# Kernel optimization log

Hardware: AMD Instinct MI355X
Metric: run time of the kernel (lower is better)

Reference implementation:

```python
import jax, jax.numpy as jnp
import numpy as np

T, B = 512, 256
OBS, H = 64, 512
M1, M2 = 512, 256


def setup_inputs() -> dict:
    key = jax.random.key(0)
    k = jax.random.split(key, 10)
    n = lambda i, shape, s=1.0: jax.random.normal(k[i], shape, dtype=jnp.float32) * s
    return {
        "x": n(0, (T * B, OBS)),
        "done": (jax.random.uniform(k[1], (T * B,)) < 0.05).astype(jnp.float32),
        "h0": n(2, (1, B, H), 0.1),
        "c0": n(3, (1, B, H), 0.1),
        "W_ih": n(4, (4 * H, OBS), OBS ** -0.5),
        "W_hh": n(5, (4 * H, H), H ** -0.5),
        "b_ih": jnp.zeros((4 * H,), jnp.float32),
        "b_hh": jnp.zeros((4 * H,), jnp.float32),
        "ln_g": jnp.ones((H,), jnp.float32),
        "ln_b": jnp.zeros((H,), jnp.float32),
        "W1": n(6, (M1, H), H ** -0.5),
        "b1": jnp.zeros((M1,), jnp.float32),
        "W2": n(7, (M2, M1), M1 ** -0.5),
        "b2": jnp.zeros((M2,), jnp.float32),
        "Wv": n(8, (1, M2), M2 ** -0.5),
        "bv": jnp.zeros((1,), jnp.float32),
    }


def _forward(x, done, h0, c0, W_ih, W_hh, b_ih, b_hh, ln_g, ln_b, W1, b1, W2, b2, Wv, bv):
    Bsz = h0.shape[1]
    obs = W_ih.shape[1]
    xs = x.reshape(-1, Bsz, obs)   # [T, B, obs]
    ds = done.reshape(-1, Bsz)     # [T, B]

    def step(carry, td):
        h, c = carry
        xt, dt = td
        m = (1.0 - dt)[:, None]    # done-based state reset, as in LSTMwithDones
        h = h * m
        c = c * m
        gates = xt @ W_ih.T + b_ih + h @ W_hh.T + b_hh  # [B, 4H]
        i, f, g, o = jnp.split(gates, 4, axis=-1)       # torch gate order i,f,g,o
        c = jax.nn.sigmoid(f) * c + jax.nn.sigmoid(i) * jnp.tanh(g)
        h = jax.nn.sigmoid(o) * jnp.tanh(c)
        return (h, c), h

    (hT, cT), hs = jax.lax.scan(step, (h0[0], c0[0]), (xs, ds))
    hidden = hs.reshape(-1, hs.shape[-1])  # flatten(cat(new_hidden), 0, 1) -> [T*B, H]

    # LayerNorm (eps = 1e-5, torch default)
    mu = hidden.mean(-1, keepdims=True)
    var = ((hidden - mu) ** 2).mean(-1, keepdims=True)
    hidden = (hidden - mu) * jax.lax.rsqrt(var + 1e-5) * ln_g + ln_b

    # MLP with tanh activation after every Linear (build_mlp appends act each layer)
    hmlp = jnp.tanh(hidden @ W1.T + b1)
    hmlp = jnp.tanh(hmlp @ W2.T + b2)
    value = hmlp @ Wv.T + bv               # [T*B, 1]
    return value, hT[None], cT[None]


def reference(x, done, h0, c0, W_ih, W_hh, b_ih, b_hh, ln_g, ln_b, W1, b1, W2, b2, Wv, bv):
    return _forward(x, done, h0, c0, W_ih, W_hh, b_ih, b_hh, ln_g, ln_b, W1, b1, W2, b2, Wv, bv)
```

## Files before the change

kernel.cpp:

```cpp
#include <hip/hip_runtime.h>
#include <stdint.h>

constexpr int T_STEPS = 512;
constexpr int BSZ     = 256;
constexpr int OBSD    = 64;
constexpr int HID     = 512;
constexpr int NROWS   = T_STEPS * BSZ;

constexpr int GROUPS = 16;
constexpr int WPG    = 16;
constexpr int BW     = 16;

typedef __attribute__((ext_vector_type(8))) short bf16x8;
typedef __attribute__((ext_vector_type(4))) float f32x4;

__device__ __forceinline__ float bf2f(uint16_t u) {
  union { uint32_t i; float f; } v; v.i = ((uint32_t)u) << 16; return v.f;
}
__device__ __forceinline__ uint16_t f2bf(float f) {
  union { float f; uint32_t i; } v; v.f = f;
  return (uint16_t)((v.i + 0x7FFFu + ((v.i >> 16) & 1u)) >> 16);
}
__device__ __forceinline__ uint64_t pack4(float a, float b, float c, float d) {
  uint32_t lo = (uint32_t)f2bf(a) | ((uint32_t)f2bf(b) << 16);
  uint32_t hi = (uint32_t)f2bf(c) | ((uint32_t)f2bf(d) << 16);
  return (uint64_t)lo | ((uint64_t)hi << 32);
}
__device__ __forceinline__ float sigm(float x) { return 1.f / (1.f + __expf(-x)); }
__device__ __forceinline__ float tanh_fast(float x) {
  float e = __expf(2.f * x);
  return 1.f - 2.f / (e + 1.f);
}

__device__ __forceinline__ void gll16(const void* g, void* l) {
  __builtin_amdgcn_global_load_lds(
      (const __attribute__((address_space(1))) uint32_t*)g,
      (__attribute__((address_space(3))) uint32_t*)l, 16, 0, 0);
}

__global__ __launch_bounds__(256, 1) void lstm_kernel(
    const float* __restrict__ xin, const float* __restrict__ done,
    const float* __restrict__ h0, const float* __restrict__ c0,
    const float* __restrict__ W_ih, const float* __restrict__ W_hh,
    const float* __restrict__ b_ih, const float* __restrict__ b_hh,
    uint16_t* __restrict__ hs, uint32_t* __restrict__ flg,
    float* __restrict__ out)
{
  __shared__ char  Ab[16 * 1152];
  __shared__ float gl[4 * 528];
  __shared__ float bl[128];

  const int wg   = blockIdx.x;
  const int g    = wg & 15;
  const int win  = wg >> 4;
  const int bg   = g * BW;
  const int tid  = threadIdx.x;
  const int lane = tid & 63;
  const int q    = tid >> 6;

  __builtin_amdgcn_fence(__ATOMIC_ACQUIRE, "agent");

  bf16x8 bq0[18], bq1[18];
  {
    const int r0  = q * 512 + win * 32 + (lane & 15);
    const int r1  = r0 + 16;
    const int kg8 = (lane >> 4) * 8;
    #pragma unroll
    for (int ks = 0; ks < 18; ++ks) {
      const float* s0 = (ks < 16)
          ? (W_hh + (size_t)r0 * 512 + ks * 32 + kg8)
          : (W_ih + (size_t)r0 * 64 + (ks - 16) * 32 + kg8);
      const float* s1 = (ks < 16)
          ? (W_hh + (size_t)r1 * 512 + ks * 32 + kg8)
          : (W_ih + (size_t)r1 * 64 + (ks - 16) * 32 + kg8);
      float4 a0 = *(const float4*)s0;
      float4 a1 = *(const float4*)(s0 + 4);
      float4 b0 = *(const float4*)s1;
      float4 b1 = *(const float4*)(s1 + 4);
      bf16x8 va, vb;
      va[0] = (short)f2bf(a0.x); va[1] = (short)f2bf(a0.y);
      va[2] = (short)f2bf(a0.z); va[3] = (short)f2bf(a0.w);
      va[4] = (short)f2bf(a1.x); va[5] = (short)f2bf(a1.y);
      va[6] = (short)f2bf(a1.z); va[7] = (short)f2bf(a1.w);
      vb[0] = (short)f2bf(b0.x); vb[1] = (short)f2bf(b0.y);
      vb[2] = (short)f2bf(b0.z); vb[3] = (short)f2bf(b0.w);
      vb[4] = (short)f2bf(b1.x); vb[5] = (short)f2bf(b1.y);
      vb[6] = (short)f2bf(b1.z); vb[7] = (short)f2bf(b1.w);
      bq0[ks] = va; bq1[ks] = vb;
    }
  }
  if (tid < 128) {
    int gq = tid >> 5, c = tid & 31;
    int grow = gq * 512 + win * 32 + c;
    bl[tid] = b_ih[grow] + b_hh[grow];
  }

  const int b_loc = tid >> 4;
  const int n0    = (tid & 15) * 2;
  float creg0 = c0[(size_t)(bg + b_loc) * HID + win * 32 + n0];
  float creg1 = c0[(size_t)(bg + b_loc) * HID + win * 32 + n0 + 1];

  const int ar  = lane & 15;
  const int kg  = lane >> 4;
  const int rw  = q * 4;

  __syncthreads();

  for (int t = 0; t < T_STEPS; ++t) {
    float dvs[4];
    #pragma unroll
    for (int r8 = 0; r8 < 4; ++r8)
      dvs[r8] = done[(size_t)t * BSZ + bg + rw + r8];
    float dv_b = done[(size_t)t * BSZ + bg + b_loc];

    const float* xrow = xin + ((size_t)t * BSZ + bg + ar) * OBSD + kg * 8;
    float4 x0a = *(const float4*)(xrow);
    float4 x0b = *(const float4*)(xrow + 4);
    float4 x1a = *(const float4*)(xrow + 32);
    float4 x1b = *(const float4*)(xrow + 36);
    bf16x8 xk0, xk1;
    xk0[0] = (short)f2bf(x0a.x); xk0[1] = (short)f2bf(x0a.y);
    xk0[2] = (short)f2bf(x0a.z); xk0[3] = (short)f2bf(x0a.w);
    xk0[4] = (short)f2bf(x0b.x); xk0[5] = (short)f2bf(x0b.y);
    xk0[6] = (short)f2bf(x0b.z); xk0[7] = (short)f2bf(x0b.w);
    xk1[0] = (short)f2bf(x1a.x); xk1[1] = (short)f2bf(x1a.y);
    xk1[2] = (short)f2bf(x1a.z); xk1[3] = (short)f2bf(x1a.w);
    xk1[4] = (short)f2bf(x1b.x); xk1[5] = (short)f2bf(x1b.y);
    xk1[6] = (short)f2bf(x1b.z); xk1[7] = (short)f2bf(x1b.w);

    f32x4 ac0 = {0.f, 0.f, 0.f, 0.f};
    f32x4 ac1 = {0.f, 0.f, 0.f, 0.f};
    ac0 = __builtin_amdgcn_mfma_f32_16x16x32_bf16(xk0, bq0[16], ac0, 0, 0, 0);
    ac1 = __builtin_amdgcn_mfma_f32_16x16x32_bf16(xk0, bq1[16], ac1, 0, 0, 0);
    ac0 = __builtin_amdgcn_mfma_f32_16x16x32_bf16(xk1, bq0[17], ac0, 0, 0, 0);
    ac1 = __builtin_amdgcn_mfma_f32_16x16x32_bf16(xk1, bq1[17], ac1, 0, 0, 0);

    if (t > 0) {
      for (;;) {
        uint32_t f = (lane < WPG)
            ? __hip_atomic_load(flg + g * 64 + q * 16 + lane,
                                __ATOMIC_RELAXED, __HIP_MEMORY_SCOPE_AGENT)
            : 0xFFFFFFFFu;
        if (__all((int)(f >= (uint32_t)t))) break;
      }
      __builtin_amdgcn_fence(__ATOMIC_ACQUIRE, "workgroup");
    }

    if (t == 0) {
      #pragma unroll
      for (int r8 = 0; r8 < 4; ++r8) {
        int r = rw + r8;
        uint64_t v0 = 0, v1 = 0;
        if (dvs[r8] <= 0.5f) {
          const float* hp = h0 + (size_t)(bg + r) * HID;
          float4 ha = *(const float4*)(hp + lane * 4);
          float4 hb = *(const float4*)(hp + 256 + lane * 4);
          v0 = pack4(ha.x, ha.y, ha.z, ha.w);
          v1 = pack4(hb.x, hb.y, hb.z, hb.w);
        }
        *(uint64_t*)(Ab + ((r * 1152 + lane * 8) ^ ((r & 7) << 4))) = v0;
        *(uint64_t*)(Ab + ((r * 1152 + 512 + lane * 8) ^ ((r & 7) << 4))) = v1;
      }
    } else {
      #pragma unroll
      for (int r8 = 0; r8 < 4; ++r8) {
        int r = rw + r8;
        const uint4* hrow =
            (const uint4*)(hs + ((size_t)(t - 1) * BSZ + bg + r) * 512);
        uint4 v = hrow[lane];
        if (dvs[r8] > 0.5f) { v.x = 0; v.y = 0; v.z = 0; v.w = 0; }
        *(uint4*)(Ab + ((r * 1152 + lane * 16) ^ ((r & 7) << 4))) = v;
      }
    }
    __syncthreads();

    #pragma unroll
    for (int ks = 0; ks < 16; ++ks) {
      int kb = ks * 64 + kg * 16;
      bf16x8 a = *(const bf16x8*)(Ab + ((ar * 1152 + kb) ^ ((ar & 7) << 4)));
      ac0 = __builtin_amdgcn_mfma_f32_16x16x32_bf16(a, bq0[ks], ac0, 0, 0, 0);
      ac1 = __builtin_amdgcn_mfma_f32_16x16x32_bf16(a, bq1[ks], ac1, 0, 0, 0);
    }
    {
      int c  = lane & 15;
      int rb = (lane >> 4) * 4;
      #pragma unroll
      for (int r = 0; r < 4; ++r) {
        gl[q * 528 + (rb + r) * 33 + c]      = ac0[r];
        gl[q * 528 + (rb + r) * 33 + 16 + c] = ac1[r];
      }
    }
    __syncthreads();

    {
      float m = dv_b > 0.5f ? 0.f : 1.f;
      float h0v, h1v;
      {
        float I = gl[b_loc * 33 + n0]          + bl[n0];
        float F = gl[528 + b_loc * 33 + n0]    + bl[32 + n0];
        float G = gl[1056 + b_loc * 33 + n0]   + bl[64 + n0];
        float O = gl[1584 + b_loc * 33 + n0]   + bl[96 + n0];
        float cc = creg0 * m;
        cc = sigm(F) * cc + sigm(I) * tanh_fast(G);
        creg0 = cc;
        h0v = sigm(O) * tanh_fast(cc);
      }
      {
        int n1 = n0 + 1;
        float I = gl[b_loc * 33 + n1]          + bl[n1];
        float F = gl[528 + b_loc * 33 + n1]    + bl[32 + n1];
        float G = gl[1056 + b_loc * 33 + n1]   + bl[64 + n1];
        float O = gl[1584 + b_loc * 33 + n1]   + bl[96 + n1];
        float cc = creg1 * m;
        cc = sigm(F) * cc + sigm(I) * tanh_fast(G);
        creg1 = cc;
        h1v = sigm(O) * tanh_fast(cc);
      }
      uint32_t pk = (uint32_t)f2bf(h0v) | ((uint32_t)f2bf(h1v) << 16);
      uint32_t* hp = (uint32_t*)(hs + ((size_t)t * BSZ + bg + b_loc) * HID + win * 32 + n0);
      __hip_atomic_store(hp, pk, __ATOMIC_RELAXED, __HIP_MEMORY_SCOPE_AGENT);
      if (t == T_STEPS - 1) {
        size_t ob = (size_t)(bg + b_loc) * HID + win * 32 + n0;
        out[NROWS + ob]         = h0v;
        out[NROWS + ob + 1]     = h1v;
        out[2 * NROWS + ob]     = creg0;
        out[2 * NROWS + ob + 1] = creg1;
      }
    }
    asm volatile("s_waitcnt vmcnt(0)" ::: "memory");
    if ((tid & 63) == 0)
      __hip_atomic_store(flg + g * 64 + q * 16 + win, (uint32_t)(t + 1),
                         __ATOMIC_RELAXED, __HIP_MEMORY_SCOPE_AGENT);
  }
}

__global__ void prep_kernel(const float* __restrict__ W1, const float* __restrict__ W2,
                            const float* __restrict__ ln_g, const float* __restrict__ ln_b,
                            const float* __restrict__ b1, uint16_t* __restrict__ dst,
                            float* __restrict__ u, float* __restrict__ v)
{
  if (blockIdx.x < 384) {
    int idx = blockIdx.x * 256 + threadIdx.x;
    int i4 = idx * 4;
    float4 val;
    if (i4 < 262144) {
      val = *(const float4*)(W1 + i4);
      int c = i4 & 511;
      float4 gv = *(const float4*)(ln_g + c);
      val.x *= gv.x; val.y *= gv.y; val.z *= gv.z; val.w *= gv.w;
    } else {
      val = *(const float4*)(W2 + (i4 - 262144));
    }
    uint32_t lo = (uint32_t)f2bf(val.x) | ((uint32_t)f2bf(val.y) << 16);
    uint32_t hi = (uint32_t)f2bf(val.z) | ((uint32_t)f2bf(val.w) << 16);
    *(uint64_t*)(dst + i4) = (uint64_t)lo | ((uint64_t)hi << 32);
  } else {
    const int lane = threadIdx.x & 63;
    const int row  = (blockIdx.x - 384) * 4 + (threadIdx.x >> 6);
    const float* wp = W1 + (size_t)row * 512 + lane * 8;
    float4 w0 = *(const float4*)wp;
    float4 w1 = *(const float4*)(wp + 4);
    float4 g0 = *(const float4*)(ln_g + lane * 8);
    float4 g1 = *(const float4*)(ln_g + lane * 8 + 4);
    float4 b0 = *(const float4*)(ln_b + lane * 8);
    float4 b1v = *(const float4*)(ln_b + lane * 8 + 4);
    float su = b0.x * w0.x + b0.y * w0.y + b0.z * w0.z + b0.w * w0.w
             + b1v.x * w1.x + b1v.y * w1.y + b1v.z * w1.z + b1v.w * w1.w;
    float sv = g0.x * w0.x + g0.y * w0.y + g0.z * w0.z + g0.w * w0.w
             + g1.x * w1.x + g1.y * w1.y + g1.z * w1.z + g1.w * w1.w;
    #pragma unroll
    for (int o = 1; o < 64; o <<= 1) { su += __shfl_xor(su, o); sv += __shfl_xor(sv, o); }
    if (lane == 0) { u[row] = su + b1[row]; v[row] = sv; }
  }
}

__global__ __launch_bounds__(256, 2) void gemm1_kernel(
    const uint16_t* __restrict__ Abase, const uint16_t* __restrict__ W,
    uint16_t* __restrict__ C,
    const float* __restrict__ uvec, const float* __restrict__ vvec)
{
  __shared__ uint16_t At[64 * 512];
  __shared__ float sRS[64];
  __shared__ float sMRS[64];
  const int tid  = threadIdx.x;
  const int lane = tid & 63;
  const int wv   = tid >> 6;
  const size_t mbase = (size_t)blockIdx.x * 64;

  for (int r8 = 0; r8 < 16; ++r8) {
    int row = wv * 16 + r8;
    int sb  = (lane * 16) ^ ((row & 7) << 4);
    gll16(Abase + (mbase + row) * 512 + sb / 2, At + row * 512);
  }
  __syncthreads();

  for (int r8 = 0; r8 < 16; ++r8) {
    int row = wv * 16 + r8;
    bf16x8 v = *(const bf16x8*)((const char*)At +
                                ((row * 1024 + lane * 16) ^ ((row & 7) << 4)));
    float s = 0.f, s2 = 0.f;
    #pragma unroll
    for (int j = 0; j < 8; ++j) {
      float f = bf2f((uint16_t)v[j]);
      s += f; s2 += f * f;
    }
    #pragma unroll
    for (int o = 1; o < 64; o <<= 1) {
      s += __shfl_xor(s, o); s2 += __shfl_xor(s2, o);
    }
    if (lane == 0) {
      float mu  = s * (1.f / 512.f);
      float var = s2 * (1.f / 512.f) - mu * mu;
      float rs  = rsqrtf(var + 1e-5f);
      sRS[row]  = rs;
      sMRS[row] = mu * rs;
    }
  }
  __syncthreads();

  const int fr = lane & 15, kg = lane >> 4;
  const int mloc = (wv & 1) * 32;
  const int nhalf = (wv >> 1) * 64;

  for (int nt = 0; nt < 4; ++nt) {
    const int nbase = nt * 128 + nhalf;
    f32x4 vz = {0.f, 0.f, 0.f, 0.f};
    f32x4 acc[4][2];
    #pragma unroll
    for (int i = 0; i < 4; ++i) { acc[i][0] = vz; acc[i][1] = vz; }

    #pragma unroll 4
    for (int kb = 0; kb < 16; ++kb) {
      const int ke = kb * 32 + kg * 8;
      bf16x8 wf[4];
      #pragma unroll
      for (int i = 0; i < 4; ++i)
        wf[i] = *(const bf16x8*)(W + (size_t)(nbase + i * 16 + fr) * 512 + ke);
      bf16x8 af[2];
      #pragma unroll
      for (int j = 0; j < 2; ++j) {
        int mr = mloc + j * 16 + fr;
        af[j] = *(const bf16x8*)((const char*)At + ((mr * 1024 + ke * 2) ^ ((mr & 7) << 4)));
      }
      #pragma unroll
      for (int i = 0; i < 4; ++i)
        #pragma unroll
        for (int j = 0; j < 2; ++j)
          acc[i][j] = __builtin_amdgcn_mfma_f32_16x16x32_bf16(wf[i], af[j], acc[i][j], 0, 0, 0);
    }

    #pragma unroll
    for (int j = 0; j < 2; ++j) {
      int ml = mloc + j * 16 + fr;
      size_t m = mbase + ml;
      float rs = sRS[ml], mrs = sMRS[ml];
      #pragma unroll
      for (int i = 0; i < 4; ++i) {
        int n = nbase + i * 16 + kg * 4;
        float4 uu = *(const float4*)(uvec + n);
        float4 vv = *(const float4*)(vvec + n);
        float o0 = tanh_fast(rs * acc[i][j][0] - mrs * vv.x + uu.x);
        float o1 = tanh_fast(rs * acc[i][j][1] - mrs * vv.y + uu.y);
        float o2 = tanh_fast(rs * acc[i][j][2] - mrs * vv.z + uu.z);
        float o3 = tanh_fast(rs * acc[i][j][3] - mrs * vv.w + uu.w);
        uint32_t lo = (uint32_t)f2bf(o0) | ((uint32_t)f2bf(o1) << 16);
        uint32_t hi = (uint32_t)f2bf(o2) | ((uint32_t)f2bf(o3) << 16);
        *(uint64_t*)(C + m * 512 + n) = (uint64_t)lo | ((uint64_t)hi << 32);
      }
    }
  }
}

__global__ __launch_bounds__(256, 2) void gemm2_value_kernel(
    const uint16_t* __restrict__ Abase, const uint16_t* __restrict__ W,
    const float* __restrict__ bias, const float* __restrict__ Wv,
    const float* __restrict__ bv, float* __restrict__ outv)
{
  __shared__ uint16_t At[64 * 512];
  __shared__ float vred[2][64];
  const int tid  = threadIdx.x;
  const int lane = tid & 63;
  const int wv   = tid >> 6;
  const size_t mbase = (size_t)blockIdx.x * 64;

  for (int r8 = 0; r8 < 16; ++r8) {
    int row = wv * 16 + r8;
    int sb  = (lane * 16) ^ ((row & 7) << 4);
    gll16(Abase + (mbase + row) * 512 + sb / 2, At + row * 512);
  }
  __syncthreads();

  const int fr = lane & 15, kg = lane >> 4;
  const int mloc = (wv & 1) * 32;
  const int nhalf = (wv >> 1) * 64;

  float vpart0 = 0.f, vpart1 = 0.f;

  #pragma unroll
  for (int nt = 0; nt < 2; ++nt) {
    const int nbase = nt * 128 + nhalf;
    f32x4 vz = {0.f, 0.f, 0.f, 0.f};
    f32x4 acc[4][2];
    #pragma unroll
    for (int i = 0; i < 4; ++i) { acc[i][0] = vz; acc[i][1] = vz; }

    #pragma unroll 4
    for (int kb = 0; kb < 16; ++kb) {
      const int ke = kb * 32 + kg * 8;
      bf16x8 wf[4];
      #pragma unroll
      for (int i = 0; i < 4; ++i)
        wf[i] = *(const bf16x8*)(W + (size_t)(nbase + i * 16 + fr) * 512 + ke);
      bf16x8 af[2];
      #pragma unroll
      for (int j = 0; j < 2; ++j) {
        int mr = mloc + j * 16 + fr;
        af[j] = *(const bf16x8*)((const char*)At + ((mr * 1024 + ke * 2) ^ ((mr & 7) << 4)));
      }
      #pragma unroll
      for (int i = 0; i < 4; ++i)
        #pragma unroll
        for (int j = 0; j < 2; ++j)
          acc[i][j] = __builtin_amdgcn_mfma_f32_16x16x32_bf16(wf[i], af[j], acc[i][j], 0, 0, 0);
    }

    #pragma unroll
    for (int j = 0; j < 2; ++j) {
      float vp = 0.f;
      #pragma unroll
      for (int i = 0; i < 4; ++i) {
        int n = nbase + i * 16 + kg * 4;
        float4 bb  = *(const float4*)(bias + n);
        float4 wv4 = *(const float4*)(Wv + n);
        vp += tanh_fast(acc[i][j][0] + bb.x) * wv4.x
            + tanh_fast(acc[i][j][1] + bb.y) * wv4.y
            + tanh_fast(acc[i][j][2] + bb.z) * wv4.z
            + tanh_fast(acc[i][j][3] + bb.w) * wv4.w;
      }
      if (j == 0) vpart0 += vp; else vpart1 += vp;
    }
  }

  vpart0 += __shfl_xor(vpart0, 16); vpart0 += __shfl_xor(vpart0, 32);
  vpart1 += __shfl_xor(vpart1, 16); vpart1 += __shfl_xor(vpart1, 32);
  if (kg == 0) {
    vred[wv >> 1][mloc + fr]      = vpart0;
    vred[wv >> 1][mloc + 16 + fr] = vpart1;
  }
  __syncthreads();
  if (tid < 64)
    outv[mbase + tid] = vred[0][tid] + vred[1][tid] + bv[0];
}

extern "C" void kernel_launch(void* const* d_in, const int* in_sizes, int n_in,
                              void* d_out, int out_size, void* d_ws, size_t ws_size,
                              hipStream_t stream)
{
  (void)in_sizes; (void)n_in;
  const float* x    = (const float*)d_in[0];
  const float* done = (const float*)d_in[1];
  const float* h0   = (const float*)d_in[2];
  const float* c0   = (const float*)d_in[3];
  const float* W_ih = (const float*)d_in[4];
  const float* W_hh = (const float*)d_in[5];
  const float* b_ih = (const float*)d_in[6];
  const float* b_hh = (const float*)d_in[7];
  const float* ln_g = (const float*)d_in[8];
  const float* ln_b = (const float*)d_in[9];
  const float* W1   = (const float*)d_in[10];
  const float* b1   = (const float*)d_in[11];
  const float* W2   = (const float*)d_in[12];
  const float* b2   = (const float*)d_in[13];
  const float* Wv   = (const float*)d_in[14];
  const float* bv   = (const float*)d_in[15];
  float* out = (float*)d_out;
  char* ws = (char*)d_ws;

  constexpr size_t NEED = 2097152ULL + 134217728ULL;
  if (ws_size < NEED) {
    hipMemsetAsync(d_out, 0, (size_t)out_size * 4, stream);
    return;
  }
  uint32_t* flg  = (uint32_t*)ws;
  uint16_t* wbf  = (uint16_t*)(ws + 16384);
  float*    uv_u = (float*)(ws + 802816);
  float*    uv_v = (float*)(ws + 802816 + 2048);
  uint16_t* hsb  = (uint16_t*)(ws + 2097152);

  hipMemsetAsync(ws, 0, 16384, stream);
  hipLaunchKernelGGL(prep_kernel, dim3(512), dim3(256), 0, stream,
                     W1, W2, ln_g, ln_b, b1, wbf, uv_u, uv_v);
  hipLaunchKernelGGL(lstm_kernel, dim3(256), dim3(256), 0, stream,
                     x, done, h0, c0, W_ih, W_hh, b_ih, b_hh, hsb, flg, out);
  hipLaunchKernelGGL(gemm1_kernel, dim3(2048), dim3(256), 0, stream,
                     hsb, wbf, hsb, uv_u, uv_v);
  hipLaunchKernelGGL(gemm2_value_kernel, dim3(2048), dim3(256), 0, stream,
                     hsb, wbf + 262144, b2, Wv, bv, out);
}
```

Before: 1.844 ms.

## Fuse MLP layer-one and layer-two GEMMs into one tail kernel via LDS

Merges the two MLP GEMM kernels into one. Layer-one activations are kept in registers as packed bf16 and written back into the shared-memory A tile, so layer two reads them from LDS instead of from a global round trip. This removes one kernel launch and the global write and re-read of the 64MB intermediate. In exchange it holds 32 packed uint64 values per thread in registers, which may raise register pressure and lower occupancy.

After: 1.843 ms. About the same (-0.0%).

```diff
diff --git a/kernel.cpp b/kernel.cpp
--- a/kernel.cpp
+++ b/kernel.cpp
@@ -274,14 +274,17 @@
   }
 }
 
-__global__ __launch_bounds__(256, 2) void gemm1_kernel(
-    const uint16_t* __restrict__ Abase, const uint16_t* __restrict__ W,
-    uint16_t* __restrict__ C,
-    const float* __restrict__ uvec, const float* __restrict__ vvec)
+__global__ __launch_bounds__(256, 2) void tail_fused_kernel(
+    const uint16_t* __restrict__ Abase, const uint16_t* __restrict__ W1b,
+    const uint16_t* __restrict__ W2b,
+    const float* __restrict__ uvec, const float* __restrict__ vvec,
+    const float* __restrict__ b2, const float* __restrict__ Wv,
+    const float* __restrict__ bv, float* __restrict__ outv)
 {
   __shared__ uint16_t At[64 * 512];
   __shared__ float sRS[64];
   __shared__ float sMRS[64];
+  __shared__ float vred[2][64];
   const int tid  = threadIdx.x;
   const int lane = tid & 63;
   const int wv   = tid >> 6;
@@ -322,6 +325,8 @@
   const int mloc = (wv & 1) * 32;
   const int nhalf = (wv >> 1) * 64;
 
+  uint64_t a1p[4][2][4];
+  #pragma unroll
   for (int nt = 0; nt < 4; ++nt) {
     const int nbase = nt * 128 + nhalf;
     f32x4 vz = {0.f, 0.f, 0.f, 0.f};
@@ -335,7 +340,7 @@
       bf16x8 wf[4];
       #pragma unroll
       for (int i = 0; i < 4; ++i)
-        wf[i] = *(const bf16x8*)(W + (size_t)(nbase + i * 16 + fr) * 512 + ke);
+        wf[i] = *(const bf16x8*)(W1b + (size_t)(nbase + i * 16 + fr) * 512 + ke);
       bf16x8 af[2];
       #pragma unroll
       for (int j = 0; j < 2; ++j) {
@@ -352,50 +357,38 @@
     #pragma unroll
     for (int j = 0; j < 2; ++j) {
       int ml = mloc + j * 16 + fr;
-      size_t m = mbase + ml;
       float rs = sRS[ml], mrs = sMRS[ml];
       #pragma unroll
       for (int i = 0; i < 4; ++i) {
         int n = nbase + i * 16 + kg * 4;
         float4 uu = *(const float4*)(uvec + n);
         float4 vv = *(const float4*)(vvec + n);
-        float o0 = tanh_fast(rs * acc[i][j][0] - mrs * vv.x + uu.x);
-        float o1 = tanh_fast(rs * acc[i][j][1] - mrs * vv.y + uu.y);
-        float o2 = tanh_fast(rs * acc[i][j][2] - mrs * vv.z + uu.z);
-        float o3 = tanh_fast(rs * acc[i][j][3] - mrs * vv.w + uu.w);
-        uint32_t lo = (uint32_t)f2bf(o0) | ((uint32_t)f2bf(o1) << 16);
-        uint32_t hi = (uint32_t)f2bf(o2) | ((uint32_t)f2bf(o3) << 16);
-        *(uint64_t*)(C + m * 512 + n) = (uint64_t)lo | ((uint64_t)hi << 32);
-      }
-    }
-  }
-}
-
-__global__ __launch_bounds__(256, 2) void gemm2_value_kernel(
-    const uint16_t* __restrict__ Abase, const uint16_t* __restrict__ W,
-    const float* __restrict__ bias, const float* __restrict__ Wv,
-    const float* __restrict__ bv, float* __restrict__ outv)
-{
-  __shared__ uint16_t At[64 * 512];
-  __shared__ float vred[2][64];
-  const int tid  = threadIdx.x;
-  const int lane = tid & 63;
-  const int wv   = tid >> 6;
-  const size_t mbase = (size_t)blockIdx.x * 64;
-
-  for (int r8 = 0; r8 < 16; ++r8) {
-    int row = wv * 16 + r8;
-    int sb  = (lane * 16) ^ ((row & 7) << 4);
-    gll16(Abase + (mbase + row) * 512 + sb / 2, At + row * 512);
-  }
-  __syncthreads();
-
-  const int fr = lane & 15, kg = lane >> 4;
-  const int mloc = (wv & 1) * 32;
-  const int nhalf = (wv >> 1) * 64;
+        a1p[nt][j][i] = pack4(
+            tanh_fast(rs * acc[i][j][0] - mrs * vv.x + uu.x),
+            tanh_fast(rs * acc[i][j][1] - mrs * vv.y + uu.y),
+            tanh_fast(rs * acc[i][j][2] - mrs * vv.z + uu.z),
+            tanh_fast(rs * acc[i][j][3] - mrs * vv.w + uu.w));
+      }
+    }
+  }
+  __syncthreads();
+
+  #pragma unroll
+  for (int nt = 0; nt < 4; ++nt) {
+    const int nbase = nt * 128 + nhalf;
+    #pragma unroll
+    for (int j = 0; j < 2; ++j) {
+      int mr = mloc + j * 16 + fr;
+      #pragma unroll
+      for (int i = 0; i < 4; ++i) {
+        int cb = (nbase + i * 16 + kg * 4) * 2;
+        *(uint64_t*)((char*)At + ((mr * 1024 + cb) ^ ((mr & 7) << 4))) = a1p[nt][j][i];
+      }
+    }
+  }
+  __syncthreads();
 
   float vpart0 = 0.f, vpart1 = 0.f;
-
   #pragma unroll
   for (int nt = 0; nt < 2; ++nt) {
     const int nbase = nt * 128 + nhalf;
@@ -410,7 +403,7 @@
       bf16x8 wf[4];
       #pragma unroll
       for (int i = 0; i < 4; ++i)
-        wf[i] = *(const bf16x8*)(W + (size_t)(nbase + i * 16 + fr) * 512 + ke);
+        wf[i] = *(const bf16x8*)(W2b + (size_t)(nbase + i * 16 + fr) * 512 + ke);
       bf16x8 af[2];
       #pragma unroll
       for (int j = 0; j < 2; ++j) {
@@ -430,7 +423,7 @@
       #pragma unroll
       for (int i = 0; i < 4; ++i) {
         int n = nbase + i * 16 + kg * 4;
-        float4 bb  = *(const float4*)(bias + n);
+        float4 bb  = *(const float4*)(b2 + n);
         float4 wv4 = *(const float4*)(Wv + n);
         vp += tanh_fast(acc[i][j][0] + bb.x) * wv4.x
             + tanh_fast(acc[i][j][1] + bb.y) * wv4.y
@@ -492,8 +485,6 @@
                      W1, W2, ln_g, ln_b, b1, wbf, uv_u, uv_v);
   hipLaunchKernelGGL(lstm_kernel, dim3(256), dim3(256), 0, stream,
                      x, done, h0, c0, W_ih, W_hh, b_ih, b_hh, hsb, flg, out);
-  hipLaunchKernelGGL(gemm1_kernel, dim3(2048), dim3(256), 0, stream,
-                     hsb, wbf, hsb, uv_u, uv_v);
-  hipLaunchKernelGGL(gemm2_value_kernel, dim3(2048), dim3(256), 0, stream,
-                     hsb, wbf + 262144, b2, Wv, bv, out);
-}
+  hipLaunchKernelGGL(tail_fused_kernel, dim3(2048), dim3(256), 0, stream,
+                     hsb, wbf, wbf + 262144, uv_u, uv_v, b2, Wv, bv, out);
+}
```
